# Performance work log

Hardware: AMD Instinct MI355X
Metric: run time of the kernel (lower is better)

Reference implementation:

```python
import jax, jax.numpy as jnp
import numpy as np
import math

N_FFT = 1024
HOP = 256
N_FRAMES = 16384
SR = 24000
FFT_BIN = N_FFT // 2 + 1
EPS = 1e-11


def hann(n):
    # torch.hann_window default (periodic=True)
    return 0.5 * (1.0 - jnp.cos(2.0 * jnp.pi * jnp.arange(n, dtype=jnp.float32) / n))


def linear_interp(x, scale):
    # x: [B, T] -> [B, T*scale]; matches F.interpolate(mode='linear', align_corners=False)
    T = x.shape[-1]
    pos = (jnp.arange(T * scale, dtype=jnp.float32) + 0.5) / scale - 0.5
    pos = jnp.clip(pos, 0.0, T - 1.0)
    lo = jnp.floor(pos).astype(jnp.int32)
    hi = jnp.minimum(lo + 1, T - 1)
    frac = pos - lo.astype(jnp.float32)
    return x[:, lo] * (1.0 - frac) + x[:, hi] * frac


def impulse_train(f0, hop_length, sample_rate):
    # f0: [B, n_frames] -> impulse train [B, n_frames*hop]
    f0_up = linear_interp(f0, hop_length)
    phase = jnp.cumsum(f0_up, axis=-1) / sample_rate
    saw = jnp.mod(phase, 1.0)
    imp = saw - jnp.roll(saw, -1, axis=-1) + f0_up / sample_rate
    # original runs under torch.no_grad()
    return jax.lax.stop_gradient(imp)


def stft(x, n_fft, hop, window):
    # torch.stft(center=True, pad_mode='reflect', onesided, normalized=False)
    pad = n_fft // 2
    xp = jnp.pad(x, ((0, 0), (pad, pad)), mode="reflect")
    nf = (xp.shape[-1] - n_fft) // hop + 1
    idx = jnp.arange(nf)[:, None] * hop + jnp.arange(n_fft)[None, :]
    frames = xp[:, idx] * window  # [B, nf, n_fft]
    return jnp.fft.rfft(frames, axis=-1).transpose(0, 2, 1)  # [B, bins, nf]


def istft(S, n_fft, hop, window):
    # torch.istft(center=True): windowed overlap-add, divide by sum of squared windows
    B = S.shape[0]
    frames = jnp.fft.irfft(S.transpose(0, 2, 1), n=n_fft, axis=-1) * window  # [B, nf, n_fft]
    nf = frames.shape[1]
    out_len = n_fft + (nf - 1) * hop
    idx = jnp.arange(nf)[:, None] * hop + jnp.arange(n_fft)[None, :]
    sig = jnp.zeros((B, out_len), frames.dtype).at[:, idx].add(frames)
    wsq = jnp.zeros((out_len,), frames.dtype).at[idx].add(
        jnp.broadcast_to(window * window, (nf, n_fft))
    )
    pad = n_fft // 2
    return sig[:, pad:-pad] / jnp.maximum(wsq[pad:-pad], EPS)


def spectral_envelope_filter(signal, envelope, n_fft, hop):
    w = hann(n_fft)
    S = stft(signal, n_fft, hop, w)[:, :, 1:]  # drop first frame -> [B, bins, n_frames]
    return istft(S * envelope, n_fft, hop, w)


def estimate_minimum_phase(amp):
    # amp: [B, bins, T] real positive envelope; cepstral min-phase along dim 1
    n = (amp.shape[1] - 1) * 2
    cep = jnp.fft.irfft(jnp.log(amp), n=n, axis=1)
    fold = jnp.concatenate(
        [jnp.ones((1,), jnp.float32),
         2.0 * jnp.ones((n // 2 - 1,), jnp.float32),
         jnp.ones((1,), jnp.float32),
         jnp.zeros((n // 2 - 1,), jnp.float32)]
    )
    cep = cep * fold[None, :, None]
    return jnp.exp(jnp.fft.rfft(cep, axis=1))  # complex min-phase spectrum [B, bins, T]


def setup_inputs() -> dict:
    key = jax.random.key(0)
    k1, k2, k3 = jax.random.split(key, 3)
    log_f0 = jnp.full((1, N_FRAMES), math.log(100.0), dtype=jnp.float32)
    spec_env_noi = jax.random.normal(k1, (1, FFT_BIN, N_FRAMES), jnp.float32) - 6.0
    spec_env_per = jax.random.normal(k2, (1, FFT_BIN, N_FRAMES), jnp.float32) - 6.0
    noise = jax.random.normal(k3, (1, HOP * N_FRAMES), jnp.float32)
    return {"log_f0": log_f0, "spec_env_noi": spec_env_noi,
            "spec_env_per": spec_env_per, "noise": noise}


def reference(log_f0, spec_env_noi, spec_env_per, noise):
    pulse = impulse_train(jnp.exp(log_f0), HOP, SR)
    noi = spectral_envelope_filter(noise, jnp.exp(spec_env_noi), N_FFT, HOP)
    per = spectral_envelope_filter(
        pulse, estimate_minimum_phase(jnp.exp(spec_env_per)), N_FFT, HOP
    )
    return noi + per  # [1, (N_FRAMES-1)*HOP]
```

## Files before the change

kernel.cpp:

```cpp
#include <hip/hip_runtime.h>
#include <math.h>

#define L_TOT 4194304
#define NFR   16384
#define OUTN  4194048


__device__ __forceinline__ int lvl_off(int a) {
  return L_TOT - (L_TOT >> (a - 1));
}

__device__ __forceinline__ int swz(int e) {
  int h = (e >> 4) & 3, g = (e >> 6) & 3, f = (e >> 8) & 3;
  return e ^ (h * 5) ^ (g * 3) ^ ((f * 12) & 15);
}

__device__ __forceinline__ int dr4(int p) {
  return ((p & 3) << 8) | (((p >> 2) & 3) << 6) | (((p >> 4) & 3) << 4) |
         (((p >> 6) & 3) << 2) | ((p >> 8) & 3);
}

__device__ __forceinline__ float f0_up_val(const float* f0arr, int j) {
  float pos = __fadd_rn(__fmul_rn(__fadd_rn((float)j, 0.5f), 1.0f / 256.0f), -0.5f);
  pos = fminf(fmaxf(pos, 0.0f), 16383.0f);
  int lo = (int)pos;
  int hi = min(lo + 1, NFR - 1);
  float frac = __fadd_rn(pos, -(float)lo);
  float a = __fmul_rn(f0arr[lo], __fadd_rn(1.0f, -frac));
  float b = __fmul_rn(f0arr[hi], frac);
  return __fadd_rn(a, b);
}

__device__ float prefix_sum(const float* W, const float* f0arr, int m) {
  float acc = 0.0f;
  bool first = true;
  int pos = 0;
  for (int a = 22; a >= 1; --a) {
    if (m & (1 << a)) {
      float node = W[lvl_off(a) + (pos >> a)];
      acc = first ? node : __fadd_rn(acc, node);
      first = false;
      pos += (1 << a);
    }
  }
  if (m & 1) {
    float node = f0_up_val(f0arr, pos);
    acc = first ? node : __fadd_rn(acc, node);
  }
  return acc;
}

__global__ __launch_bounds__(256) void init_tables(const float* __restrict__ logf0,
                                                   float* __restrict__ W) {
  int g = blockIdx.x * 256 + threadIdx.x;
  float* twc = W + 2 * L_TOT;
  float* tws = twc + 512;
  float* wh  = twc + 1024;
  float* f0arr = twc + 2048;
  if (g < 512) {
    double a = (double)g * 3.14159265358979323846 / 512.0;
    twc[g] = (float)cos(a);
    tws[g] = (float)sin(a);
  }
  if (g < 1024) {
    double a = (double)g * 3.14159265358979323846 / 512.0;
    wh[g] = (float)(0.5 - 0.5 * cos(a));
  }
  if (g >= 2048 && g < 2048 + NFR) {
    f0arr[g - 2048] = (float)exp((double)logf0[g - 2048]);
  }
}

__global__ __launch_bounds__(256) void tree_kernel(float* W) {
  const float* f0arr = W + 2 * L_TOT + 2048;
  __shared__ float A[2048];
  __shared__ float B[1024];
  int tid = threadIdx.x;
  int base = blockIdx.x * 2048;
  for (int i = tid; i < 2048; i += 256) A[i] = f0_up_val(f0arr, base + i);
  __syncthreads();
  float* src = A;
  float* dst = B;
  int cnt = 1024;
  for (int a = 1; a <= 11; ++a) {
    int gbase = base >> a;
    for (int i = tid; i < cnt; i += 256) {
      float v = __fadd_rn(src[2 * i], src[2 * i + 1]);
      dst[i] = v;
      if (a == 11) W[lvl_off(11) + gbase + i] = v;
    }
    __syncthreads();
    float* tmp = src; src = dst; dst = tmp;
    cnt >>= 1;
  }
}

__global__ __launch_bounds__(256) void tree_top_kernel(float* W) {
  __shared__ float A[2048];
  __shared__ float B[1024];
  int tid = threadIdx.x;
  for (int i = tid; i < 2048; i += 256) A[i] = W[lvl_off(11) + i];
  __syncthreads();
  float* src = A;
  float* dst = B;
  int cnt = 1024;
  for (int a = 12; a <= 22; ++a) {
    for (int i = tid; i < cnt; i += 256) {
      float v = __fadd_rn(src[2 * i], src[2 * i + 1]);
      dst[i] = v;
      W[lvl_off(a) + i] = v;
    }
    __syncthreads();
    float* tmp = src; src = dst; dst = tmp;
    cnt >>= 1;
  }
}

__global__ __launch_bounds__(256) void pulse_kernel(float* W) {
  const float* f0arr = W + 2 * L_TOT + 2048;
  __shared__ float Tl[510];
  __shared__ float P[4100];
  int tid = threadIdx.x;
  int base = blockIdx.x * 4096;

  float v[16];
#pragma unroll
  for (int c = 0; c < 16; ++c) v[c] = f0_up_val(f0arr, base + 16 * tid + c);
  float s2[8], s4[4], s8[2];
#pragma unroll
  for (int j = 0; j < 8; ++j) s2[j] = __fadd_rn(v[2 * j], v[2 * j + 1]);
#pragma unroll
  for (int j = 0; j < 4; ++j) s4[j] = __fadd_rn(s2[2 * j], s2[2 * j + 1]);
  s8[0] = __fadd_rn(s4[0], s4[1]);
  s8[1] = __fadd_rn(s4[2], s4[3]);
  Tl[tid] = __fadd_rn(s8[0], s8[1]);
  __syncthreads();
  if (tid < 128) Tl[256 + tid] = __fadd_rn(Tl[2 * tid], Tl[2 * tid + 1]);
  __syncthreads();
  if (tid < 64)  Tl[384 + tid] = __fadd_rn(Tl[256 + 2 * tid], Tl[256 + 2 * tid + 1]);
  __syncthreads();
  if (tid < 32)  Tl[448 + tid] = __fadd_rn(Tl[384 + 2 * tid], Tl[384 + 2 * tid + 1]);
  __syncthreads();
  if (tid < 16)  Tl[480 + tid] = __fadd_rn(Tl[448 + 2 * tid], Tl[448 + 2 * tid + 1]);
  __syncthreads();
  if (tid < 8)   Tl[496 + tid] = __fadd_rn(Tl[480 + 2 * tid], Tl[480 + 2 * tid + 1]);
  __syncthreads();
  if (tid < 4)   Tl[504 + tid] = __fadd_rn(Tl[496 + 2 * tid], Tl[496 + 2 * tid + 1]);
  __syncthreads();
  if (tid < 2)   Tl[508 + tid] = __fadd_rn(Tl[504 + 2 * tid], Tl[504 + 2 * tid + 1]);
  __syncthreads();

  float accT = 0.0f;
  bool firstT = true;
  {
    int pos = 0;
    for (int a = 22; a >= 12; --a) {
      if (base & (1 << a)) {
        float node = W[lvl_off(a) + (pos >> a)];
        accT = firstT ? node : __fadd_rn(accT, node);
        firstT = false;
        pos += (1 << a);
      }
    }
  }
  float accM = accT;
  bool firstM = firstT;
  {
    int rh = 16 * tid;
    int lpos = 0;
    for (int a = 11; a >= 4; --a) {
      if (rh & (1 << a)) {
        float node = Tl[512 - (512 >> (a - 4)) + (lpos >> a)];
        accM = firstM ? node : __fadd_rn(accM, node);
        firstM = false;
        lpos += (1 << a);
      }
    }
  }
  if (tid >= 1) P[16 * tid] = accM;
#pragma unroll
  for (int c = 1; c <= 15; ++c) {
    float acc = accM;
    bool first = firstM;
    int lp = 0;
    if (c & 8) { float n = s8[lp >> 3]; acc = first ? n : __fadd_rn(acc, n); first = false; lp += 8; }
    if (c & 4) { float n = s4[lp >> 2]; acc = first ? n : __fadd_rn(acc, n); first = false; lp += 4; }
    if (c & 2) { float n = s2[lp >> 1]; acc = first ? n : __fadd_rn(acc, n); first = false; lp += 2; }
    if (c & 1) { float n = v[lp];       acc = first ? n : __fadd_rn(acc, n); }
    P[16 * tid + c] = acc;
  }
  if (tid == 0) P[4096] = prefix_sum(W, f0arr, base + 4096);
  if (tid == 1) {
    int m2 = base + 4097;
    P[4097] = (m2 <= L_TOT) ? prefix_sum(W, f0arr, m2) : 0.0f;
  }
  __syncthreads();

  float o[16];
#pragma unroll
  for (int c = 0; c < 16; ++c) {
    int i = base + 16 * tid + c;
    float P1 = P[16 * tid + c + 1];
    float P2 = (i == L_TOT - 1) ? prefix_sum(W, f0arr, 1)
                                : P[16 * tid + c + 2];
    float t1 = __fdiv_rn(P1, 24000.0f);
    float saw1 = __fadd_rn(t1, -floorf(t1));
    float t2 = __fdiv_rn(P2, 24000.0f);
    float saw2 = __fadd_rn(t2, -floorf(t2));
    float cc = __fdiv_rn(v[c], 24000.0f);
    o[c] = __fadd_rn(__fadd_rn(saw1, -saw2), cc);
  }
#pragma unroll
  for (int k = 0; k < 4; ++k)
    *(float4*)&W[L_TOT + base + 16 * tid + 4 * k] =
        make_float4(o[4 * k], o[4 * k + 1], o[4 * k + 2], o[4 * k + 3]);
}


template <int DIR>
__device__ __forceinline__ void bfly_dif(float2* F, int base, int L, float ur, float ui) {
  if (DIR < 0) ui = -ui;
  int e0 = swz(base), e1 = swz(base + L), e2 = swz(base + 2 * L), e3 = swz(base + 3 * L);
  float2 x0 = F[e0], x1 = F[e1], x2 = F[e2], x3 = F[e3];
  float s0r = x0.x + x2.x, s0i = x0.y + x2.y;
  float s1r = x1.x + x3.x, s1i = x1.y + x3.y;
  float d0r = x0.x - x2.x, d0i = x0.y - x2.y;
  float ddr = x1.x - x3.x, ddi = x1.y - x3.y;
  float t3r = (DIR > 0) ? -ddi : ddi;
  float t3i = (DIR > 0) ? ddr : -ddr;
  float vr = ur * ur - ui * ui, vi = 2.0f * ur * ui;
  float w3r = ur * vr - ui * vi, w3i = ur * vi + ui * vr;
  F[e0] = make_float2(s0r + s1r, s0i + s1i);
  float a1r = d0r + t3r, a1i = d0i + t3i;
  F[e1] = make_float2(a1r * ur - a1i * ui, a1r * ui + a1i * ur);
  float a2r = s0r - s1r, a2i = s0i - s1i;
  F[e2] = make_float2(a2r * vr - a2i * vi, a2r * vi + a2i * vr);
  float a3r = d0r - t3r, a3i = d0i - t3i;
  F[e3] = make_float2(a3r * w3r - a3i * w3i, a3r * w3i + a3i * w3r);
  __syncthreads();
}

template <int DIR>
__device__ __forceinline__ void bfly_dit(float2* F, int base, int L, float ur, float ui) {
  if (DIR < 0) ui = -ui;
  int e0 = swz(base), e1 = swz(base + L), e2 = swz(base + 2 * L), e3 = swz(base + 3 * L);
  float2 x0 = F[e0], x1 = F[e1], x2 = F[e2], x3 = F[e3];
  float vr = ur * ur - ui * ui, vi = 2.0f * ur * ui;
  float w3r = ur * vr - ui * vi, w3i = ur * vi + ui * vr;
  float b1r = x1.x * ur - x1.y * ui, b1i = x1.x * ui + x1.y * ur;
  float b2r = x2.x * vr - x2.y * vi, b2i = x2.x * vi + x2.y * vr;
  float b3r = x3.x * w3r - x3.y * w3i, b3i = x3.x * w3i + x3.y * w3r;
  float s0r = x0.x + b2r, s0i = x0.y + b2i;
  float d0r = x0.x - b2r, d0i = x0.y - b2i;
  float s1r = b1r + b3r, s1i = b1i + b3i;
  float ddr = b1r - b3r, ddi = b1i - b3i;
  float d1r = (DIR > 0) ? -ddi : ddi;
  float d1i = (DIR > 0) ? ddr : -ddr;
  F[e0] = make_float2(s0r + s1r, s0i + s1i);
  F[e1] = make_float2(d0r + d1r, d0i + d1i);
  F[e2] = make_float2(s0r - s1r, s0i - s1i);
  F[e3] = make_float2(d0r - d1r, d0i - d1i);
  __syncthreads();
}

template <int DIR>
__device__ __forceinline__ void fft_dif(float2* F, int tid, const float2* T0,
                                        const float2* T1, const float2* T2,
                                        const float2* T3) {
  __syncthreads();
  float2 t;
  t = T0[tid];      bfly_dif<DIR>(F, tid, 256, t.x, t.y);
  t = T1[tid & 63]; bfly_dif<DIR>(F, ((tid >> 6) << 8) | (tid & 63), 64, t.x, t.y);
  t = T2[tid & 15]; bfly_dif<DIR>(F, ((tid >> 4) << 6) | (tid & 15), 16, t.x, t.y);
  t = T3[tid & 3];  bfly_dif<DIR>(F, ((tid >> 2) << 4) | (tid & 3), 4, t.x, t.y);
  bfly_dif<DIR>(F, tid << 2, 1, 1.0f, 0.0f);
}

template <int DIR>
__device__ __forceinline__ void fft_dit(float2* F, int tid, const float2* T0,
                                        const float2* T1, const float2* T2,
                                        const float2* T3) {
  __syncthreads();
  float2 t;
  bfly_dit<DIR>(F, tid << 2, 1, 1.0f, 0.0f);
  t = T3[tid & 3];  bfly_dit<DIR>(F, ((tid >> 2) << 4) | (tid & 3), 4, t.x, t.y);
  t = T2[tid & 15]; bfly_dit<DIR>(F, ((tid >> 4) << 6) | (tid & 15), 16, t.x, t.y);
  t = T1[tid & 63]; bfly_dit<DIR>(F, ((tid >> 6) << 8) | (tid & 63), 64, t.x, t.y);
  t = T0[tid];      bfly_dit<DIR>(F, tid, 256, t.x, t.y);
}

__device__ __forceinline__ float hann_w(int i, const float2* T0) {
  int j = (i > 512) ? (1024 - i) : i;
  float c = (j <= 256) ? T0[j].x : -T0[512 - j].x;
  return 0.5f - 0.5f * c;
}

__device__ __forceinline__ void combine_one(int k, float An, const float2* F, float2* H) {
  int k2 = (1024 - k) & 1023;
  float2 z = F[swz(dr4(k))], mm = F[swz(dr4(k2))];
  float Ar = 0.5f * (z.x + mm.x), Ai = 0.5f * (z.y - mm.y);
  float Br = 0.5f * (z.y + mm.y), Bi = 0.5f * (mm.x - z.x);
  float2 h = H[k];
  H[k] = make_float2(Br * h.x - Bi * h.y + Ar * An,
                     Br * h.y + Bi * h.x + Ai * An);
}

__global__ __launch_bounds__(256) void column_kernel(
    const float* __restrict__ noise,
    const float* __restrict__ envn,
    const float* __restrict__ envp,
    const float* __restrict__ W,
    float* __restrict__ out) {
  __shared__ float2 F[1024];
  __shared__ float2 hA[513], hB[513];
  __shared__ float2 TW[341];
  int tid = threadIdx.x;
  int bid = blockIdx.x;
  int g = (bid & 7) * 1024 + (bid >> 3);
  int fA = 2 * g;
  const float* pulse = W + L_TOT;
  const float* gtab = W + 2 * L_TOT;
  const float2* T0 = TW;
  const float2* T1 = TW + 257;
  const float2* T2 = TW + 321;
  const float2* T3 = TW + 337;

  for (int i = tid; i < 341; i += 256) {
    int e;
    if (i < 257) e = i;
    else if (i < 321) e = (i - 257) << 2;
    else if (i < 337) e = (i - 321) << 4;
    else e = (i - 337) << 6;
    TW[i] = make_float2(gtab[e], gtab[512 + e]);
  }
  for (int k = tid; k < 513; k += 256) {
    float2 e = *(const float2*)&envp[k * NFR + fA];
    hA[k] = e;
  }
  __syncthreads();

#pragma unroll
  for (int j = 0; j < 4; ++j) {
    int i = tid + 256 * j;
    int k = (i <= 512) ? i : 1024 - i;
    F[swz(i)] = hA[k];
  }
  fft_dif<+1>(F, tid, T0, T1, T2, T3);
#pragma unroll
  for (int j = 0; j < 4; ++j) {
    int p = tid + 256 * j;
    int k = dr4(p);
    float sc = ((k & 511) == 0) ? (1.0f / 1024.0f)
                                : ((k < 512) ? (2.0f / 1024.0f) : 0.0f);
    int e = swz(p);
    float2 a = F[e];
    F[e] = make_float2(a.x * sc, a.y * sc);
  }
  fft_dit<-1>(F, tid, T0, T1, T2, T3);
  for (int k = tid; k < 513; k += 256) {
    int k2 = (1024 - k) & 1023;
    float2 z = F[swz(k)], mm = F[swz(k2)];
    float GAr = 0.5f * (z.x + mm.x), GAi = 0.5f * (z.y - mm.y);
    float GBr = 0.5f * (z.y + mm.y), GBi = 0.5f * (mm.x - z.x);
    float er = expf(GAr);
    float si, co;
    sincosf(GAi, &si, &co);
    hA[k] = make_float2(er * co, er * si);
    er = expf(GBr);
    sincosf(GBi, &si, &co);
    hB[k] = make_float2(er * co, er * si);
  }
  __syncthreads();

#define PACK_FRAME(QOFF, J)                                            \
  {                                                                    \
    int i = tid + 256 * (J);                                           \
    int q = (QOFF) + i;                                                \
    if (q < 0) q = -q;                                                 \
    else if (q >= L_TOT) q = 2 * L_TOT - 2 - q;                        \
    float wv = hann_w(i, T0);                                          \
    F[swz(i)] = make_float2(noise[q] * wv, pulse[q] * wv);             \
  }
  PACK_FRAME(256 * fA - 256, 0)
  PACK_FRAME(256 * fA - 256, 1)
  PACK_FRAME(256 * fA - 256, 2)
  PACK_FRAME(256 * fA - 256, 3)
  fft_dif<-1>(F, tid, T0, T1, T2, T3);
  float2 eA0 = *(const float2*)&envn[tid * NFR + fA];
  combine_one(tid, expf(eA0.x), F, hA);
  float2 eA1 = *(const float2*)&envn[(tid + 256) * NFR + fA];
  combine_one(tid + 256, expf(eA1.x), F, hA);
  float2 eA2 = make_float2(0.0f, 0.0f);
  if (tid == 0) {
    eA2 = *(const float2*)&envn[512 * NFR + fA];
    combine_one(512, expf(eA2.x), F, hA);
  }
  __syncthreads();

  PACK_FRAME(256 * fA, 0)
  PACK_FRAME(256 * fA, 1)
  PACK_FRAME(256 * fA, 2)
  PACK_FRAME(256 * fA, 3)
  fft_dif<-1>(F, tid, T0, T1, T2, T3);
  combine_one(tid, expf(eA0.y), F, hB);
  combine_one(tid + 256, expf(eA1.y), F, hB);
  if (tid == 0) combine_one(512, expf(eA2.y), F, hB);
  __syncthreads();

#pragma unroll
  for (int j = 0; j < 4; ++j) {
    int i = tid + 256 * j;
    float2 zv;
    if (i <= 512) {
      zv = make_float2(hA[i].x - hB[i].y, hA[i].y + hB[i].x);
    } else {
      int jj = 1024 - i;
      zv = make_float2(hA[jj].x + hB[jj].y, hB[jj].x - hA[jj].y);
    }
    F[swz(dr4(i))] = zv;
  }
  fft_dit<+1>(F, tid, T0, T1, T2, T3);
  const float scl = 1.0f / 1536.0f;
  {
    float2 f0v = F[swz(tid)];
    float2 f1v = F[swz(tid + 256)];
    float2 f2v = F[swz(tid + 512)];
    float2 f3v = F[swz(tid + 768)];
    float hw0 = hann_w(tid, T0) * scl;
    float hw1 = hann_w(tid + 256, T0) * scl;
    float hw2 = hann_w(tid + 512, T0) * scl;
    float hw3 = hann_w(tid + 768, T0) * scl;
    int tb = 256 * fA - 512 + tid;
    float val;
    val = f0v.x * hw0;
    if (tb >= 0) atomicAdd(&out[tb], val);
    val = f1v.x * hw1 + f0v.y * hw0;
    if (tb + 256 >= 0 && tb + 256 < OUTN) atomicAdd(&out[tb + 256], val);
    val = f2v.x * hw2 + f1v.y * hw1;
    if (tb + 512 < OUTN) atomicAdd(&out[tb + 512], val);
    val = f3v.x * hw3 + f2v.y * hw2;
    if (tb + 768 < OUTN) atomicAdd(&out[tb + 768], val);
    val = f3v.y * hw3;
    if (tb + 1024 < OUTN) atomicAdd(&out[tb + 1024], val);
  }
#undef PACK_FRAME
}

__global__ __launch_bounds__(256) void finalize_kernel(float* __restrict__ out,
                                                       const float* __restrict__ W) {
  const float* wh = W + 2 * L_TOT + 1024;
  int tid = threadIdx.x;
  int t = (blockIdx.x == 0) ? tid : (OUTN - 256 + tid);
  int p = t + 512;
  int jmin = max(0, (p - 768) >> 8);
  int jmax = min(NFR - 1, p >> 8);
  float wsq = 0.0f;
  for (int j = jmin; j <= jmax; ++j) {
    float w = wh[p - 256 * j];
    wsq += w * w;
  }
  out[t] = out[t] * (1.5f / fmaxf(wsq, 1e-11f));
}

extern "C" void kernel_launch(void* const* d_in, const int* in_sizes, int n_in,
                              void* d_out, int out_size, void* d_ws, size_t ws_size,
                              hipStream_t stream) {
  const float* logf0 = (const float*)d_in[0];
  const float* envn  = (const float*)d_in[1];
  const float* envp  = (const float*)d_in[2];
  const float* noise = (const float*)d_in[3];
  float* out = (float*)d_out;
  float* W = (float*)d_ws;

  init_tables<<<dim3(72), dim3(256), 0, stream>>>(logf0, W);
  tree_kernel<<<dim3(2048), dim3(256), 0, stream>>>(W);
  tree_top_kernel<<<dim3(1), dim3(256), 0, stream>>>(W);
  pulse_kernel<<<dim3(L_TOT / 4096), dim3(256), 0, stream>>>(W);
  hipMemsetAsync(d_out, 0, (size_t)out_size * sizeof(float), stream);
  column_kernel<<<dim3(NFR / 2), dim3(256), 0, stream>>>(noise, envn, envp, W, out);
  finalize_kernel<<<dim3(2), dim3(256), 0, stream>>>(out, W);
}
```

Baseline: 238.6 us.

## Fuse table init into tree kernel, precompute block prefixes, merge finalize into column

Table setup now runs inside the tree kernel, and each tree block recomputes its f0 values locally from logf0. The block-boundary prefix sums move into tree_top_kernel, so each pulse block loads two precomputed values instead of walking the tree. The finalize kernel goes away: the edge window-square normalization is applied before the atomic adds in the column kernel. The FFT stages hoist swizzled addresses, and the cepstrum fold scaling is fused into the last DIF stage. Together this removes two launches and some serial per-block work, at the cost of heavier code in the column kernel.

After: 244.0 us. 1.02x slower.

```diff
diff --git a/kernel.cpp b/kernel.cpp
--- a/kernel.cpp
+++ b/kernel.cpp
@@ -28,6 +28,17 @@
   float frac = __fadd_rn(pos, -(float)lo);
   float a = __fmul_rn(f0arr[lo], __fadd_rn(1.0f, -frac));
   float b = __fmul_rn(f0arr[hi], frac);
+  return __fadd_rn(a, b);
+}
+
+__device__ __forceinline__ float f0_up_local(const float* Fl, int w0, int j) {
+  float pos = __fadd_rn(__fmul_rn(__fadd_rn((float)j, 0.5f), 1.0f / 256.0f), -0.5f);
+  pos = fminf(fmaxf(pos, 0.0f), 16383.0f);
+  int lo = (int)pos;
+  int hi = min(lo + 1, NFR - 1);
+  float frac = __fadd_rn(pos, -(float)lo);
+  float a = __fmul_rn(Fl[lo - w0], __fadd_rn(1.0f, -frac));
+  float b = __fmul_rn(Fl[hi - w0], frac);
   return __fadd_rn(a, b);
 }
 
@@ -50,34 +61,34 @@
   return acc;
 }
 
-__global__ __launch_bounds__(256) void init_tables(const float* __restrict__ logf0,
+__global__ __launch_bounds__(256) void tree_kernel(const float* __restrict__ logf0,
                                                    float* __restrict__ W) {
-  int g = blockIdx.x * 256 + threadIdx.x;
-  float* twc = W + 2 * L_TOT;
-  float* tws = twc + 512;
-  float* wh  = twc + 1024;
-  float* f0arr = twc + 2048;
-  if (g < 512) {
-    double a = (double)g * 3.14159265358979323846 / 512.0;
-    twc[g] = (float)cos(a);
-    tws[g] = (float)sin(a);
-  }
-  if (g < 1024) {
-    double a = (double)g * 3.14159265358979323846 / 512.0;
-    wh[g] = (float)(0.5 - 0.5 * cos(a));
-  }
-  if (g >= 2048 && g < 2048 + NFR) {
-    f0arr[g - 2048] = (float)exp((double)logf0[g - 2048]);
-  }
-}
-
-__global__ __launch_bounds__(256) void tree_kernel(float* W) {
-  const float* f0arr = W + 2 * L_TOT + 2048;
+  int tid = threadIdx.x;
+  if (blockIdx.x < 72) {
+    int g = blockIdx.x * 256 + tid;
+    float* twc = W + 2 * L_TOT;
+    float* tws = twc + 512;
+    float* f0arr = twc + 2048;
+    if (g < 512) {
+      double a = (double)g * 3.14159265358979323846 / 512.0;
+      twc[g] = (float)cos(a);
+      tws[g] = (float)sin(a);
+    }
+    if (g >= 2048 && g < 2048 + NFR) {
+      f0arr[g - 2048] = (float)exp((double)logf0[g - 2048]);
+    }
+  }
+  __shared__ float Fl[10];
   __shared__ float A[2048];
   __shared__ float B[1024];
-  int tid = threadIdx.x;
   int base = blockIdx.x * 2048;
-  for (int i = tid; i < 2048; i += 256) A[i] = f0_up_val(f0arr, base + i);
+  int w0 = (base >> 8) - 1;
+  if (tid < 10) {
+    int f = min(max(w0 + tid, 0), NFR - 1);
+    Fl[tid] = (float)exp((double)logf0[f]);
+  }
+  __syncthreads();
+  for (int i = tid; i < 2048; i += 256) A[i] = f0_up_local(Fl, w0, base + i);
   __syncthreads();
   float* src = A;
   float* dst = B;
@@ -113,6 +124,12 @@
     __syncthreads();
     float* tmp = src; src = dst; dst = tmp;
     cnt >>= 1;
+  }
+  const float* f0arr = W + 2 * L_TOT + 2048;
+  for (int b = tid; b < 1024; b += 256) {
+    W[2 * b] = prefix_sum(W, f0arr, 4096 * (b + 1));
+    int m2 = 4096 * b + 4097;
+    W[2 * b + 1] = (m2 <= L_TOT) ? prefix_sum(W, f0arr, m2) : 0.0f;
   }
 }
 
@@ -189,11 +206,8 @@
     if (c & 1) { float n = v[lp];       acc = first ? n : __fadd_rn(acc, n); }
     P[16 * tid + c] = acc;
   }
-  if (tid == 0) P[4096] = prefix_sum(W, f0arr, base + 4096);
-  if (tid == 1) {
-    int m2 = base + 4097;
-    P[4097] = (m2 <= L_TOT) ? prefix_sum(W, f0arr, m2) : 0.0f;
-  }
+  if (tid == 0) P[4096] = W[2 * blockIdx.x];
+  if (tid == 1) P[4097] = W[2 * blockIdx.x + 1];
   __syncthreads();
 
   float o[16];
@@ -216,11 +230,10 @@
         make_float4(o[4 * k], o[4 * k + 1], o[4 * k + 2], o[4 * k + 3]);
 }
 
-
 template <int DIR>
-__device__ __forceinline__ void bfly_dif(float2* F, int base, int L, float ur, float ui) {
+__device__ __forceinline__ void bfly_dif(float2* F, int e0, int e1, int e2, int e3,
+                                         float ur, float ui) {
   if (DIR < 0) ui = -ui;
-  int e0 = swz(base), e1 = swz(base + L), e2 = swz(base + 2 * L), e3 = swz(base + 3 * L);
   float2 x0 = F[e0], x1 = F[e1], x2 = F[e2], x3 = F[e3];
   float s0r = x0.x + x2.x, s0i = x0.y + x2.y;
   float s1r = x1.x + x3.x, s1i = x1.y + x3.y;
@@ -241,9 +254,9 @@
 }
 
 template <int DIR>
-__device__ __forceinline__ void bfly_dit(float2* F, int base, int L, float ur, float ui) {
+__device__ __forceinline__ void bfly_dit(float2* F, int e0, int e1, int e2, int e3,
+                                         float ur, float ui) {
   if (DIR < 0) ui = -ui;
-  int e0 = swz(base), e1 = swz(base + L), e2 = swz(base + 2 * L), e3 = swz(base + 3 * L);
   float2 x0 = F[e0], x1 = F[e1], x2 = F[e2], x3 = F[e3];
   float vr = ur * ur - ui * ui, vi = 2.0f * ur * ui;
   float w3r = ur * vr - ui * vi, w3i = ur * vi + ui * vr;
@@ -263,36 +276,22 @@
   __syncthreads();
 }
 
-template <int DIR>
-__device__ __forceinline__ void fft_dif(float2* F, int tid, const float2* T0,
-                                        const float2* T1, const float2* T2,
-                                        const float2* T3) {
-  __syncthreads();
-  float2 t;
-  t = T0[tid];      bfly_dif<DIR>(F, tid, 256, t.x, t.y);
-  t = T1[tid & 63]; bfly_dif<DIR>(F, ((tid >> 6) << 8) | (tid & 63), 64, t.x, t.y);
-  t = T2[tid & 15]; bfly_dif<DIR>(F, ((tid >> 4) << 6) | (tid & 15), 16, t.x, t.y);
-  t = T3[tid & 3];  bfly_dif<DIR>(F, ((tid >> 2) << 4) | (tid & 3), 4, t.x, t.y);
-  bfly_dif<DIR>(F, tid << 2, 1, 1.0f, 0.0f);
-}
-
-template <int DIR>
-__device__ __forceinline__ void fft_dit(float2* F, int tid, const float2* T0,
-                                        const float2* T1, const float2* T2,
-                                        const float2* T3) {
-  __syncthreads();
-  float2 t;
-  bfly_dit<DIR>(F, tid << 2, 1, 1.0f, 0.0f);
-  t = T3[tid & 3];  bfly_dit<DIR>(F, ((tid >> 2) << 4) | (tid & 3), 4, t.x, t.y);
-  t = T2[tid & 15]; bfly_dit<DIR>(F, ((tid >> 4) << 6) | (tid & 15), 16, t.x, t.y);
-  t = T1[tid & 63]; bfly_dit<DIR>(F, ((tid >> 6) << 8) | (tid & 63), 64, t.x, t.y);
-  t = T0[tid];      bfly_dit<DIR>(F, tid, 256, t.x, t.y);
-}
-
 __device__ __forceinline__ float hann_w(int i, const float2* T0) {
   int j = (i > 512) ? (1024 - i) : i;
   float c = (j <= 256) ? T0[j].x : -T0[512 - j].x;
   return 0.5f - 0.5f * c;
+}
+
+__device__ __forceinline__ float edge_scale(int t, const float2* T0) {
+  int p = t + 512;
+  int jmin = max(0, (p - 768) >> 8);
+  int jmax = min(NFR - 1, p >> 8);
+  float wsq = 0.0f;
+  for (int j = jmin; j <= jmax; ++j) {
+    float w = hann_w(p - 256 * j, T0);
+    wsq += w * w;
+  }
+  return 1.5f / fmaxf(wsq, 1e-11f);
 }
 
 __device__ __forceinline__ void combine_one(int k, float An, const float2* F, float2* H) {
@@ -337,55 +336,112 @@
     float2 e = *(const float2*)&envp[k * NFR + fA];
     hA[k] = e;
   }
-  __syncthreads();
-
-#pragma unroll
-  for (int j = 0; j < 4; ++j) {
-    int i = tid + 256 * j;
-    int k = (i <= 512) ? i : 1024 - i;
-    F[swz(i)] = hA[k];
-  }
-  fft_dif<+1>(F, tid, T0, T1, T2, T3);
-#pragma unroll
-  for (int j = 0; j < 4; ++j) {
-    int p = tid + 256 * j;
-    int k = dr4(p);
-    float sc = ((k & 511) == 0) ? (1.0f / 1024.0f)
-                                : ((k < 512) ? (2.0f / 1024.0f) : 0.0f);
-    int e = swz(p);
-    float2 a = F[e];
-    F[e] = make_float2(a.x * sc, a.y * sc);
-  }
-  fft_dit<-1>(F, tid, T0, T1, T2, T3);
-  for (int k = tid; k < 513; k += 256) {
-    int k2 = (1024 - k) & 1023;
-    float2 z = F[swz(k)], mm = F[swz(k2)];
+
+  int a00 = swz(tid), a01 = swz(tid + 256), a02 = swz(tid + 512), a03 = swz(tid + 768);
+  int b1_ = ((tid >> 6) << 8) | (tid & 63);
+  int a10 = swz(b1_), a11 = swz(b1_ + 64), a12 = swz(b1_ + 128), a13 = swz(b1_ + 192);
+  int b2_ = ((tid >> 4) << 6) | (tid & 15);
+  int a20 = swz(b2_), a21 = swz(b2_ + 16), a22 = swz(b2_ + 32), a23 = swz(b2_ + 48);
+  int b3_ = ((tid >> 2) << 4) | (tid & 3);
+  int a30 = swz(b3_), a31 = swz(b3_ + 4), a32 = swz(b3_ + 8), a33 = swz(b3_ + 12);
+  int q_ = tid << 2;
+  int a40 = swz(q_), a41 = swz(q_ + 1), a42 = swz(q_ + 2), a43 = swz(q_ + 3);
+  __syncthreads();
+
+  F[a00] = hA[tid];
+  F[a01] = hA[tid + 256];
+  F[a02] = (tid == 0) ? hA[512] : hA[512 - tid];
+  F[a03] = hA[256 - tid];
+  __syncthreads();
+  { float2 t_ = T0[tid];      bfly_dif<+1>(F, a00, a01, a02, a03, t_.x, t_.y); }
+  { float2 t_ = T1[tid & 63]; bfly_dif<+1>(F, a10, a11, a12, a13, t_.x, t_.y); }
+  { float2 t_ = T2[tid & 15]; bfly_dif<+1>(F, a20, a21, a22, a23, t_.x, t_.y); }
+  { float2 t_ = T3[tid & 3];  bfly_dif<+1>(F, a30, a31, a32, a33, t_.x, t_.y); }
+  {
+    int drt = ((tid & 3) << 6) | (((tid >> 2) & 3) << 4) |
+              (((tid >> 4) & 3) << 2) | ((tid >> 6) & 3);
+    float2 x0 = F[a40], x1 = F[a41], x2 = F[a42], x3 = F[a43];
+    float s0r = x0.x + x2.x, s0i = x0.y + x2.y;
+    float s1r = x1.x + x3.x, s1i = x1.y + x3.y;
+    float d0r = x0.x - x2.x, d0i = x0.y - x2.y;
+    float ddr = x1.x - x3.x, ddi = x1.y - x3.y;
+    float y0r = s0r + s1r, y0i = s0i + s1i;
+    float y1r = d0r - ddi, y1i = d0i + ddr;
+    float y2r = s0r - s1r, y2i = s0i - s1i;
+    float sc0 = (drt == 0) ? (1.0f / 1024.0f) : (2.0f / 1024.0f);
+    float sc2 = (drt == 0) ? (1.0f / 1024.0f) : 0.0f;
+    y0r *= sc0; y0i *= sc0;
+    y1r *= (2.0f / 1024.0f); y1i *= (2.0f / 1024.0f);
+    y2r *= sc2; y2i *= sc2;
+    float S0r = y0r + y2r, S0i = y0i + y2i;
+    float D0r = y0r - y2r, D0i = y0i - y2i;
+    float D1r = y1i, D1i = -y1r;
+    F[a40] = make_float2(S0r + y1r, S0i + y1i);
+    F[a41] = make_float2(D0r + D1r, D0i + D1i);
+    F[a42] = make_float2(S0r - y1r, S0i - y1i);
+    F[a43] = make_float2(D0r - D1r, D0i - D1i);
+  }
+  __syncthreads();
+  { float2 t_ = T3[tid & 3];  bfly_dit<-1>(F, a30, a31, a32, a33, t_.x, t_.y); }
+  { float2 t_ = T2[tid & 15]; bfly_dit<-1>(F, a20, a21, a22, a23, t_.x, t_.y); }
+  { float2 t_ = T1[tid & 63]; bfly_dit<-1>(F, a10, a11, a12, a13, t_.x, t_.y); }
+  { float2 t_ = T0[tid];      bfly_dit<-1>(F, a00, a01, a02, a03, t_.x, t_.y); }
+  {
+    int k2 = (1024 - tid) & 1023;
+    float2 z = F[a00], mm = F[swz(k2)];
     float GAr = 0.5f * (z.x + mm.x), GAi = 0.5f * (z.y - mm.y);
     float GBr = 0.5f * (z.y + mm.y), GBi = 0.5f * (mm.x - z.x);
     float er = expf(GAr);
     float si, co;
     sincosf(GAi, &si, &co);
-    hA[k] = make_float2(er * co, er * si);
+    hA[tid] = make_float2(er * co, er * si);
     er = expf(GBr);
     sincosf(GBi, &si, &co);
-    hB[k] = make_float2(er * co, er * si);
-  }
-  __syncthreads();
-
-#define PACK_FRAME(QOFF, J)                                            \
+    hB[tid] = make_float2(er * co, er * si);
+
+    z = F[a01]; mm = F[swz(768 - tid)];
+    GAr = 0.5f * (z.x + mm.x); GAi = 0.5f * (z.y - mm.y);
+    GBr = 0.5f * (z.y + mm.y); GBi = 0.5f * (mm.x - z.x);
+    er = expf(GAr);
+    sincosf(GAi, &si, &co);
+    hA[tid + 256] = make_float2(er * co, er * si);
+    er = expf(GBr);
+    sincosf(GBi, &si, &co);
+    hB[tid + 256] = make_float2(er * co, er * si);
+
+    if (tid == 0) {
+      z = F[a02];
+      GAr = 0.5f * (z.x + z.x); GAi = 0.0f;
+      GBr = 0.5f * (z.y + z.y); GBi = 0.0f;
+      er = expf(GAr);
+      sincosf(GAi, &si, &co);
+      hA[512] = make_float2(er * co, er * si);
+      er = expf(GBr);
+      sincosf(GBi, &si, &co);
+      hB[512] = make_float2(er * co, er * si);
+    }
+  }
+  __syncthreads();
+
+#define PACK_FRAME(QOFF, J, ADDR)                                      \
   {                                                                    \
     int i = tid + 256 * (J);                                           \
     int q = (QOFF) + i;                                                \
     if (q < 0) q = -q;                                                 \
     else if (q >= L_TOT) q = 2 * L_TOT - 2 - q;                        \
     float wv = hann_w(i, T0);                                          \
-    F[swz(i)] = make_float2(noise[q] * wv, pulse[q] * wv);             \
-  }
-  PACK_FRAME(256 * fA - 256, 0)
-  PACK_FRAME(256 * fA - 256, 1)
-  PACK_FRAME(256 * fA - 256, 2)
-  PACK_FRAME(256 * fA - 256, 3)
-  fft_dif<-1>(F, tid, T0, T1, T2, T3);
+    F[ADDR] = make_float2(noise[q] * wv, pulse[q] * wv);               \
+  }
+  PACK_FRAME(256 * fA - 256, 0, a00)
+  PACK_FRAME(256 * fA - 256, 1, a01)
+  PACK_FRAME(256 * fA - 256, 2, a02)
+  PACK_FRAME(256 * fA - 256, 3, a03)
+  __syncthreads();
+  { float2 t_ = T0[tid];      bfly_dif<-1>(F, a00, a01, a02, a03, t_.x, t_.y); }
+  { float2 t_ = T1[tid & 63]; bfly_dif<-1>(F, a10, a11, a12, a13, t_.x, t_.y); }
+  { float2 t_ = T2[tid & 15]; bfly_dif<-1>(F, a20, a21, a22, a23, t_.x, t_.y); }
+  { float2 t_ = T3[tid & 3];  bfly_dif<-1>(F, a30, a31, a32, a33, t_.x, t_.y); }
+  bfly_dif<-1>(F, a40, a41, a42, a43, 1.0f, 0.0f);
   float2 eA0 = *(const float2*)&envn[tid * NFR + fA];
   combine_one(tid, expf(eA0.x), F, hA);
   float2 eA1 = *(const float2*)&envn[(tid + 256) * NFR + fA];
@@ -397,11 +453,16 @@
   }
   __syncthreads();
 
-  PACK_FRAME(256 * fA, 0)
-  PACK_FRAME(256 * fA, 1)
-  PACK_FRAME(256 * fA, 2)
-  PACK_FRAME(256 * fA, 3)
-  fft_dif<-1>(F, tid, T0, T1, T2, T3);
+  PACK_FRAME(256 * fA, 0, a00)
+  PACK_FRAME(256 * fA, 1, a01)
+  PACK_FRAME(256 * fA, 2, a02)
+  PACK_FRAME(256 * fA, 3, a03)
+  __syncthreads();
+  { float2 t_ = T0[tid];      bfly_dif<-1>(F, a00, a01, a02, a03, t_.x, t_.y); }
+  { float2 t_ = T1[tid & 63]; bfly_dif<-1>(F, a10, a11, a12, a13, t_.x, t_.y); }
+  { float2 t_ = T2[tid & 15]; bfly_dif<-1>(F, a20, a21, a22, a23, t_.x, t_.y); }
+  { float2 t_ = T3[tid & 3];  bfly_dif<-1>(F, a30, a31, a32, a33, t_.x, t_.y); }
+  bfly_dif<-1>(F, a40, a41, a42, a43, 1.0f, 0.0f);
   combine_one(tid, expf(eA0.y), F, hB);
   combine_one(tid + 256, expf(eA1.y), F, hB);
   if (tid == 0) combine_one(512, expf(eA2.y), F, hB);
@@ -419,47 +480,54 @@
     }
     F[swz(dr4(i))] = zv;
   }
-  fft_dit<+1>(F, tid, T0, T1, T2, T3);
+  __syncthreads();
+  bfly_dit<+1>(F, a40, a41, a42, a43, 1.0f, 0.0f);
+  { float2 t_ = T3[tid & 3];  bfly_dit<+1>(F, a30, a31, a32, a33, t_.x, t_.y); }
+  { float2 t_ = T2[tid & 15]; bfly_dit<+1>(F, a20, a21, a22, a23, t_.x, t_.y); }
+  { float2 t_ = T1[tid & 63]; bfly_dit<+1>(F, a10, a11, a12, a13, t_.x, t_.y); }
+  { float2 t_ = T0[tid];      bfly_dit<+1>(F, a00, a01, a02, a03, t_.x, t_.y); }
   const float scl = 1.0f / 1536.0f;
   {
-    float2 f0v = F[swz(tid)];
-    float2 f1v = F[swz(tid + 256)];
-    float2 f2v = F[swz(tid + 512)];
-    float2 f3v = F[swz(tid + 768)];
+    float2 f0v = F[a00], f1v = F[a01], f2v = F[a02], f3v = F[a03];
     float hw0 = hann_w(tid, T0) * scl;
     float hw1 = hann_w(tid + 256, T0) * scl;
     float hw2 = hann_w(tid + 512, T0) * scl;
     float hw3 = hann_w(tid + 768, T0) * scl;
     int tb = 256 * fA - 512 + tid;
     float val;
+    int t;
+    t = tb;
     val = f0v.x * hw0;
-    if (tb >= 0) atomicAdd(&out[tb], val);
+    if (t >= 0) {
+      if (t < 256) val *= edge_scale(t, T0);
+      atomicAdd(&out[t], val);
+    }
+    t = tb + 256;
     val = f1v.x * hw1 + f0v.y * hw0;
-    if (tb + 256 >= 0 && tb + 256 < OUTN) atomicAdd(&out[tb + 256], val);
+    if (t >= 0 && t < OUTN) {
+      if (t < 256 || t >= OUTN - 256) val *= edge_scale(t, T0);
+      atomicAdd(&out[t], val);
+    }
+    t = tb + 512;
     val = f2v.x * hw2 + f1v.y * hw1;
-    if (tb + 512 < OUTN) atomicAdd(&out[tb + 512], val);
+    if (t < OUTN) {
+      if (t < 256 || t >= OUTN - 256) val *= edge_scale(t, T0);
+      atomicAdd(&out[t], val);
+    }
+    t = tb + 768;
     val = f3v.x * hw3 + f2v.y * hw2;
-    if (tb + 768 < OUTN) atomicAdd(&out[tb + 768], val);
+    if (t < OUTN) {
+      if (t >= OUTN - 256) val *= edge_scale(t, T0);
+      atomicAdd(&out[t], val);
+    }
+    t = tb + 1024;
     val = f3v.y * hw3;
-    if (tb + 1024 < OUTN) atomicAdd(&out[tb + 1024], val);
+    if (t < OUTN) {
+      if (t >= OUTN - 256) val *= edge_scale(t, T0);
+      atomicAdd(&out[t], val);
+    }
   }
 #undef PACK_FRAME
-}
-
-__global__ __launch_bounds__(256) void finalize_kernel(float* __restrict__ out,
-                                                       const float* __restrict__ W) {
-  const float* wh = W + 2 * L_TOT + 1024;
-  int tid = threadIdx.x;
-  int t = (blockIdx.x == 0) ? tid : (OUTN - 256 + tid);
-  int p = t + 512;
-  int jmin = max(0, (p - 768) >> 8);
-  int jmax = min(NFR - 1, p >> 8);
-  float wsq = 0.0f;
-  for (int j = jmin; j <= jmax; ++j) {
-    float w = wh[p - 256 * j];
-    wsq += w * w;
-  }
-  out[t] = out[t] * (1.5f / fmaxf(wsq, 1e-11f));
 }
 
 extern "C" void kernel_launch(void* const* d_in, const int* in_sizes, int n_in,
@@ -472,11 +540,9 @@
   float* out = (float*)d_out;
   float* W = (float*)d_ws;
 
-  init_tables<<<dim3(72), dim3(256), 0, stream>>>(logf0, W);
-  tree_kernel<<<dim3(2048), dim3(256), 0, stream>>>(W);
+  tree_kernel<<<dim3(2048), dim3(256), 0, stream>>>(logf0, W);
   tree_top_kernel<<<dim3(1), dim3(256), 0, stream>>>(W);
   pulse_kernel<<<dim3(L_TOT / 4096), dim3(256), 0, stream>>>(W);
   hipMemsetAsync(d_out, 0, (size_t)out_size * sizeof(float), stream);
   column_kernel<<<dim3(NFR / 2), dim3(256), 0, stream>>>(noise, envn, envp, W, out);
-  finalize_kernel<<<dim3(2), dim3(256), 0, stream>>>(out, W);
-}
+}
```
